# Optimization experiments

Hardware: AMD Instinct MI355X
Metric: run time of the kernel (lower is better)

Reference implementation:

```python
import jax, jax.numpy as jnp
import numpy as np

N_BITS = 8
QMAX = float(2 ** (N_BITS - 1) - 1)   # 127
QMIN = -QMAX - 1.0                     # -128
EPS = 1e-8


def _fq(x, scale):
    # symmetric fake quant: round, clamp, dequant
    return jnp.clip(jnp.round(x / scale), QMIN, QMAX) * scale


def fake_quant_per_token(x):
    # one scale per [..., :] vector (amax over last dim)
    max_abs = jnp.max(jnp.abs(x), axis=-1, keepdims=True)
    scale = jnp.maximum(max_abs / QMAX, EPS)
    return _fq(x, scale)


def fake_quant_per_channel(w):
    # w: [out, in]; ch_axis=0 -> one scale per output row (reduce over dim 1)
    max_abs = jnp.max(jnp.abs(w), axis=1, keepdims=True)
    scale = jnp.maximum(max_abs / QMAX, EPS)
    return _fq(w, scale)


def setup_inputs() -> dict:
    key = jax.random.key(0)
    kx, kw, kb = jax.random.split(key, 3)
    B, S, D_IN, D_OUT = 4, 2048, 4096, 4096
    x = jax.random.normal(kx, (B, S, D_IN), dtype=jnp.float32)
    w = jax.random.normal(kw, (D_OUT, D_IN), dtype=jnp.float32) * 0.02
    b = jax.random.normal(kb, (D_OUT,), dtype=jnp.float32) * 0.02
    return {"x": x, "w": w, "b": b}


def reference(x, w, b):
    # fake-quant path: W8 per-channel weight, A8 per-token activation
    w_q = fake_quant_per_channel(w)           # [O, I]
    x_q = fake_quant_per_token(x)             # [B, S, I]
    y = jnp.einsum('bsi,oi->bso', x_q, w_q) + b
    return y
```

## Files before the change

### kernel.cpp

```cpp
#include <hip/hip_runtime.h>
#include <hip/hip_bf16.h>


#define K_DIM 4096
#define N_DIM 4096
#define NT (K_DIM / 128)

typedef int v4i __attribute__((ext_vector_type(4)));

__device__ __forceinline__ void cp16(void* lds, const void* g) {
    __builtin_amdgcn_global_load_lds(
        (const __attribute__((address_space(1))) void*)g,
        (__attribute__((address_space(3))) void*)lds, 16, 0, 0);
}

__global__ __launch_bounds__(256) void quant_rows_kernel(
    const float* __restrict__ x, const float* __restrict__ w, int M,
    char* __restrict__ qx, char* __restrict__ qw,
    float* __restrict__ sx, float* __restrict__ sw) {
    const int blk = blockIdx.x;
    const bool is_x = blk < M;
    const int row = is_x ? blk : blk - M;
    const float* rp = (is_x ? x : w) + (size_t)row * 4096;
    char* qdst = is_x ? qx : qw;
    float* sdst = is_x ? sx : sw;

    const int tid = threadIdx.x;

    float4 v[4];
#pragma unroll
    for (int i = 0; i < 4; ++i)
        v[i] = *(const float4*)(rp + 4 * (tid + 256 * i));

    float m = 0.0f;
#pragma unroll
    for (int i = 0; i < 4; ++i) {
        m = fmaxf(m, fmaxf(fmaxf(fabsf(v[i].x), fabsf(v[i].y)),
                           fmaxf(fabsf(v[i].z), fabsf(v[i].w))));
    }
#pragma unroll
    for (int off = 32; off > 0; off >>= 1)
        m = fmaxf(m, __shfl_down(m, off));

    __shared__ float red[4];
    if ((tid & 63) == 0) red[tid >> 6] = m;
    __syncthreads();
    const float amax = fmaxf(fmaxf(red[0], red[1]), fmaxf(red[2], red[3]));
    const float scale = fmaxf(amax / 127.0f, 1e-8f);

    int* qout = (int*)(qdst + (size_t)row * 4096);
#pragma unroll
    for (int i = 0; i < 4; ++i) {
        int q0 = (int)fminf(fmaxf(rintf(v[i].x / scale), -128.0f), 127.0f);
        int q1 = (int)fminf(fmaxf(rintf(v[i].y / scale), -128.0f), 127.0f);
        int q2 = (int)fminf(fmaxf(rintf(v[i].z / scale), -128.0f), 127.0f);
        int q3 = (int)fminf(fmaxf(rintf(v[i].w / scale), -128.0f), 127.0f);
        qout[tid + 256 * i] =
            (q0 & 255) | ((q1 & 255) << 8) | ((q2 & 255) << 16) | ((q3 & 255) << 24);
    }
    if (tid == 0) sdst[row] = scale;
}

__global__ __launch_bounds__(512, 2) void gemm_i8_kernel(
    const char* __restrict__ qx, const char* __restrict__ qw,
    const float* __restrict__ sx, const float* __restrict__ sw,
    const float* __restrict__ bias, float* __restrict__ y) {

    __shared__ __align__(16) char lds[131072];

    const int tid  = threadIdx.x;
    const int wave = tid >> 6;
    const int lane = tid & 63;
    const int ln   = lane & 15;
    const int lg   = lane >> 4;
    const int wm   = wave >> 2;
    const int wn   = wave & 3;

    const int bm = blockIdx.y;
    const int bn = blockIdx.x;

    const int ci0 = tid,       r0s = ci0 >> 3, c0s = (ci0 & 7) ^ (r0s & 7);
    const int ci1 = tid + 512, r1s = ci1 >> 3, c1s = (ci1 & 7) ^ (r1s & 7);
    const char* aS0 = qx + (size_t)(bm * 256 + r0s) * K_DIM + c0s * 16;
    const char* aS1 = qx + (size_t)(bm * 256 + r1s) * K_DIM + c1s * 16;
    const char* bS0 = qw + (size_t)(bn * 256 + r0s) * K_DIM + c0s * 16;
    const char* bS1 = qw + (size_t)(bn * 256 + r1s) * K_DIM + c1s * 16;
    const int ldsC0 = ci0 * 16, ldsC1 = ci1 * 16;

#define SLOT_A(par, h) ((par) * 65536 + (h) * 16384)
#define SLOT_B(par, h) ((par) * 65536 + 32768 + (h) * 16384)
#define STAGE_A(par, h, t) do {                                              \
    cp16(lds + SLOT_A(par, h) + ldsC0,                                       \
         aS0 + (size_t)(h) * 128 * K_DIM + (size_t)(t) * 128);               \
    cp16(lds + SLOT_A(par, h) + ldsC1,                                       \
         aS1 + (size_t)(h) * 128 * K_DIM + (size_t)(t) * 128); } while (0)
#define STAGE_B(par, h, t) do {                                              \
    cp16(lds + SLOT_B(par, h) + ldsC0,                                       \
         bS0 + (size_t)(h) * 128 * K_DIM + (size_t)(t) * 128);               \
    cp16(lds + SLOT_B(par, h) + ldsC1,                                       \
         bS1 + (size_t)(h) * 128 * K_DIM + (size_t)(t) * 128); } while (0)

    const int ch0 = (lg ^ (ln & 7)) * 16;
    const int ch1 = ch0 ^ 64;
    const int aRd = wm * 16384 + ln * 128;
    const int bRd = 32768 + (wn >> 1) * 16384 + ((wn & 1) * 64 + ln) * 128;

    v4i acc[8][4] = {};

    STAGE_A(0, 0, 0); STAGE_A(0, 1, 0);
    STAGE_B(0, 0, 0); STAGE_B(0, 1, 0);
    STAGE_B(1, 0, 1); STAGE_B(1, 1, 1);
    asm volatile("s_waitcnt vmcnt(4)" ::: "memory");
    __builtin_amdgcn_s_barrier();
    asm volatile("" ::: "memory");

    for (int t = 0; t < NT; ++t) {
        const int par  = t & 1;
        const int base = par * 65536;
        v4i afr[4], bfr[4];

#pragma unroll
        for (int m = 0; m < 4; ++m)
            afr[m] = *(const v4i*)(lds + base + aRd + m * 2048 + ch0);
#pragma unroll
        for (int n = 0; n < 4; ++n)
            bfr[n] = *(const v4i*)(lds + base + bRd + n * 2048 + ch0);
        if (t + 1 < NT) STAGE_A(par ^ 1, 0, t + 1);
        __builtin_amdgcn_s_barrier();
        asm volatile("" ::: "memory");
        __builtin_amdgcn_s_setprio(1);
#pragma unroll
        for (int m = 0; m < 4; ++m)
#pragma unroll
            for (int n = 0; n < 4; ++n)
                acc[m][n] = __builtin_amdgcn_mfma_i32_16x16x64_i8(
                    afr[m], bfr[n], acc[m][n], 0, 0, 0);
        __builtin_amdgcn_s_setprio(0);
        __builtin_amdgcn_s_barrier();
        asm volatile("" ::: "memory");

#pragma unroll
        for (int m = 0; m < 4; ++m)
            afr[m] = *(const v4i*)(lds + base + aRd + (4 + m) * 2048 + ch0);
        if (t + 1 < NT) STAGE_A(par ^ 1, 1, t + 1);
        __builtin_amdgcn_s_barrier();
        asm volatile("" ::: "memory");
        __builtin_amdgcn_s_setprio(1);
#pragma unroll
        for (int m = 0; m < 4; ++m)
#pragma unroll
            for (int n = 0; n < 4; ++n)
                acc[4 + m][n] = __builtin_amdgcn_mfma_i32_16x16x64_i8(
                    afr[m], bfr[n], acc[4 + m][n], 0, 0, 0);
        __builtin_amdgcn_s_setprio(0);
        __builtin_amdgcn_s_barrier();
        asm volatile("" ::: "memory");

#pragma unroll
        for (int m = 0; m < 4; ++m)
            afr[m] = *(const v4i*)(lds + base + aRd + m * 2048 + ch1);
#pragma unroll
        for (int n = 0; n < 4; ++n)
            bfr[n] = *(const v4i*)(lds + base + bRd + n * 2048 + ch1);
        __builtin_amdgcn_s_barrier();
        asm volatile("" ::: "memory");
        __builtin_amdgcn_s_setprio(1);
#pragma unroll
        for (int m = 0; m < 4; ++m)
#pragma unroll
            for (int n = 0; n < 4; ++n)
                acc[m][n] = __builtin_amdgcn_mfma_i32_16x16x64_i8(
                    afr[m], bfr[n], acc[m][n], 0, 0, 0);
        __builtin_amdgcn_s_setprio(0);
        __builtin_amdgcn_s_barrier();
        asm volatile("" ::: "memory");

#pragma unroll
        for (int m = 0; m < 4; ++m)
            afr[m] = *(const v4i*)(lds + base + aRd + (4 + m) * 2048 + ch1);
        if (t + 2 < NT) { STAGE_B(par, 0, t + 2); STAGE_B(par, 1, t + 2); }
        __builtin_amdgcn_s_barrier();
        asm volatile("" ::: "memory");
        __builtin_amdgcn_s_setprio(1);
#pragma unroll
        for (int m = 0; m < 4; ++m)
#pragma unroll
            for (int n = 0; n < 4; ++n)
                acc[4 + m][n] = __builtin_amdgcn_mfma_i32_16x16x64_i8(
                    afr[m], bfr[n], acc[4 + m][n], 0, 0, 0);
        __builtin_amdgcn_s_setprio(0);
        if (t + 2 < NT)
            asm volatile("s_waitcnt vmcnt(4)" ::: "memory");
        else
            asm volatile("s_waitcnt vmcnt(0)" ::: "memory");
        __builtin_amdgcn_s_barrier();
        asm volatile("" ::: "memory");
    }

    const int m_base = bm * 256 + wm * 128;
    const int n_base = bn * 256 + wn * 64;

    float sxr[8][4];
#pragma unroll
    for (int m = 0; m < 8; ++m)
#pragma unroll
        for (int r = 0; r < 4; ++r)
            sxr[m][r] = sx[m_base + m * 16 + lg * 4 + r];

#pragma unroll
    for (int n = 0; n < 4; ++n) {
        const int col = n_base + n * 16 + ln;
        const float swv = sw[col];
        const float bv  = bias[col];
#pragma unroll
        for (int m = 0; m < 8; ++m) {
            const int row = m_base + m * 16 + lg * 4;
#pragma unroll
            for (int r = 0; r < 4; ++r) {
                y[(size_t)(row + r) * N_DIM + col] =
                    (float)acc[m][n][r] * sxr[m][r] * swv + bv;
            }
        }
    }
#undef SLOT_A
#undef SLOT_B
#undef STAGE_A
#undef STAGE_B
}

extern "C" void kernel_launch(void* const* d_in, const int* in_sizes, int n_in,
                              void* d_out, int out_size, void* d_ws, size_t ws_size,
                              hipStream_t stream) {
    const float* x = (const float*)d_in[0];
    const float* w = (const float*)d_in[1];
    const float* b = (const float*)d_in[2];
    float* y = (float*)d_out;

    const int M = in_sizes[0] / K_DIM;
    const int O = in_sizes[1] / K_DIM;

    char* qx = (char*)d_ws;
    char* qw = qx + (size_t)M * K_DIM;
    float* sx = (float*)(qw + (size_t)O * K_DIM);
    float* sw = sx + M;

    quant_rows_kernel<<<M + O, 256, 0, stream>>>(x, w, M, qx, qw, sx, sw);

    dim3 grid(N_DIM / 256, M / 256);
    gemm_i8_kernel<<<grid, 512, 0, stream>>>(qx, qw, sx, sw, b, y);
}
```

Baseline: 385.9 us.

## Restructure int8 GEMM main loop with register double-buffered fragments and swapped A/B prefetch

The main K loop is reorganised so LDS fragment reads for the next MFMA phase are issued before the current phase's MFMAs. The first fragment of the next tile is loaded at the end of the current iteration using separate aA/aB/b0/b1 register sets. The global-to-LDS prefetch is reordered: A is now prefetched two tiles ahead and B one tile ahead. sched_barrier calls pin instruction order around the barriers. This aims to hide LDS latency behind MFMA work, but adds register pressure and a full vmcnt(0) wait each iteration, which may expose global load latency.

```diff
diff --git a/kernel.cpp b/kernel.cpp
--- a/kernel.cpp
+++ b/kernel.cpp
@@ -100,101 +100,111 @@
     cp16(lds + SLOT_B(par, h) + ldsC1,                                       \
          bS1 + (size_t)(h) * 128 * K_DIM + (size_t)(t) * 128); } while (0)
 
+#define BAR()  __builtin_amdgcn_s_barrier()
+#define FENCE() asm volatile("" ::: "memory")
+#define SCHED() __builtin_amdgcn_sched_barrier(0)
+
     const int ch0 = (lg ^ (ln & 7)) * 16;
     const int ch1 = ch0 ^ 64;
     const int aRd = wm * 16384 + ln * 128;
     const int bRd = 32768 + (wn >> 1) * 16384 + ((wn & 1) * 64 + ln) * 128;
 
     v4i acc[8][4] = {};
+    v4i aA[4], aB[4], b0[4], b1[4];
 
     STAGE_A(0, 0, 0); STAGE_A(0, 1, 0);
     STAGE_B(0, 0, 0); STAGE_B(0, 1, 0);
-    STAGE_B(1, 0, 1); STAGE_B(1, 1, 1);
+    STAGE_A(1, 0, 1); STAGE_A(1, 1, 1);
     asm volatile("s_waitcnt vmcnt(4)" ::: "memory");
-    __builtin_amdgcn_s_barrier();
-    asm volatile("" ::: "memory");
+    BAR(); FENCE();
+#pragma unroll
+    for (int m = 0; m < 4; ++m)
+        aA[m] = *(const v4i*)(lds + aRd + m * 2048 + ch0);
+#pragma unroll
+    for (int n = 0; n < 4; ++n)
+        b0[n] = *(const v4i*)(lds + bRd + n * 2048 + ch0);
 
     for (int t = 0; t < NT; ++t) {
-        const int par  = t & 1;
-        const int base = par * 65536;
-        v4i afr[4], bfr[4];
-
-#pragma unroll
-        for (int m = 0; m < 4; ++m)
-            afr[m] = *(const v4i*)(lds + base + aRd + m * 2048 + ch0);
+        const int par   = t & 1;
+        const int base  = par << 16;
+        const int baseN = base ^ 65536;
+
+#pragma unroll
+        for (int m = 0; m < 4; ++m)
+            aB[m] = *(const v4i*)(lds + base + aRd + (4 + m) * 2048 + ch0);
+        if (t + 1 < NT) { STAGE_B(par ^ 1, 0, t + 1); STAGE_B(par ^ 1, 1, t + 1); }
+        SCHED();
+        BAR(); FENCE();
+        SCHED();
+        __builtin_amdgcn_s_setprio(1);
+#pragma unroll
+        for (int m = 0; m < 4; ++m)
+#pragma unroll
+            for (int n = 0; n < 4; ++n)
+                acc[m][n] = __builtin_amdgcn_mfma_i32_16x16x64_i8(
+                    aA[m], b0[n], acc[m][n], 0, 0, 0);
+        __builtin_amdgcn_s_setprio(0);
+        BAR(); FENCE();
+
+#pragma unroll
+        for (int m = 0; m < 4; ++m)
+            aA[m] = *(const v4i*)(lds + base + aRd + m * 2048 + ch1);
 #pragma unroll
         for (int n = 0; n < 4; ++n)
-            bfr[n] = *(const v4i*)(lds + base + bRd + n * 2048 + ch0);
-        if (t + 1 < NT) STAGE_A(par ^ 1, 0, t + 1);
-        __builtin_amdgcn_s_barrier();
-        asm volatile("" ::: "memory");
+            b1[n] = *(const v4i*)(lds + base + bRd + n * 2048 + ch1);
+        SCHED();
+        BAR(); FENCE();
+        SCHED();
+        __builtin_amdgcn_s_setprio(1);
+#pragma unroll
+        for (int m = 0; m < 4; ++m)
+#pragma unroll
+            for (int n = 0; n < 4; ++n)
+                acc[4 + m][n] = __builtin_amdgcn_mfma_i32_16x16x64_i8(
+                    aB[m], b0[n], acc[4 + m][n], 0, 0, 0);
+        __builtin_amdgcn_s_setprio(0);
+        BAR(); FENCE();
+
+#pragma unroll
+        for (int m = 0; m < 4; ++m)
+            aB[m] = *(const v4i*)(lds + base + aRd + (4 + m) * 2048 + ch1);
+        SCHED();
+        BAR(); FENCE();
+        SCHED();
         __builtin_amdgcn_s_setprio(1);
 #pragma unroll
         for (int m = 0; m < 4; ++m)
 #pragma unroll
             for (int n = 0; n < 4; ++n)
                 acc[m][n] = __builtin_amdgcn_mfma_i32_16x16x64_i8(
-                    afr[m], bfr[n], acc[m][n], 0, 0, 0);
-        __builtin_amdgcn_s_setprio(0);
-        __builtin_amdgcn_s_barrier();
-        asm volatile("" ::: "memory");
-
-#pragma unroll
-        for (int m = 0; m < 4; ++m)
-            afr[m] = *(const v4i*)(lds + base + aRd + (4 + m) * 2048 + ch0);
-        if (t + 1 < NT) STAGE_A(par ^ 1, 1, t + 1);
-        __builtin_amdgcn_s_barrier();
-        asm volatile("" ::: "memory");
+                    aA[m], b1[n], acc[m][n], 0, 0, 0);
+        __builtin_amdgcn_s_setprio(0);
+        asm volatile("s_waitcnt lgkmcnt(0)" ::: "memory");
+        asm volatile("s_waitcnt vmcnt(0)" ::: "memory");
+        BAR(); FENCE();
+
+        if (t + 1 < NT) {
+#pragma unroll
+            for (int m = 0; m < 4; ++m)
+                aA[m] = *(const v4i*)(lds + baseN + aRd + m * 2048 + ch0);
+#pragma unroll
+            for (int n = 0; n < 4; ++n)
+                b0[n] = *(const v4i*)(lds + baseN + bRd + n * 2048 + ch0);
+        }
+        SCHED();
+        BAR(); FENCE();
+        SCHED();
         __builtin_amdgcn_s_setprio(1);
 #pragma unroll
         for (int m = 0; m < 4; ++m)
 #pragma unroll
             for (int n = 0; n < 4; ++n)
                 acc[4 + m][n] = __builtin_amdgcn_mfma_i32_16x16x64_i8(
-                    afr[m], bfr[n], acc[4 + m][n], 0, 0, 0);
-        __builtin_amdgcn_s_setprio(0);
-        __builtin_amdgcn_s_barrier();
-        asm volatile("" ::: "memory");
-
-#pragma unroll
-        for (int m = 0; m < 4; ++m)
-            afr[m] = *(const v4i*)(lds + base + aRd + m * 2048 + ch1);
-#pragma unroll
-        for (int n = 0; n < 4; ++n)
-            bfr[n] = *(const v4i*)(lds + base + bRd + n * 2048 + ch1);
-        __builtin_amdgcn_s_barrier();
-        asm volatile("" ::: "memory");
-        __builtin_amdgcn_s_setprio(1);
-#pragma unroll
-        for (int m = 0; m < 4; ++m)
-#pragma unroll
-            for (int n = 0; n < 4; ++n)
-                acc[m][n] = __builtin_amdgcn_mfma_i32_16x16x64_i8(
-                    afr[m], bfr[n], acc[m][n], 0, 0, 0);
-        __builtin_amdgcn_s_setprio(0);
-        __builtin_amdgcn_s_barrier();
-        asm volatile("" ::: "memory");
-
-#pragma unroll
-        for (int m = 0; m < 4; ++m)
-            afr[m] = *(const v4i*)(lds + base + aRd + (4 + m) * 2048 + ch1);
-        if (t + 2 < NT) { STAGE_B(par, 0, t + 2); STAGE_B(par, 1, t + 2); }
-        __builtin_amdgcn_s_barrier();
-        asm volatile("" ::: "memory");
-        __builtin_amdgcn_s_setprio(1);
-#pragma unroll
-        for (int m = 0; m < 4; ++m)
-#pragma unroll
-            for (int n = 0; n < 4; ++n)
-                acc[4 + m][n] = __builtin_amdgcn_mfma_i32_16x16x64_i8(
-                    afr[m], bfr[n], acc[4 + m][n], 0, 0, 0);
-        __builtin_amdgcn_s_setprio(0);
-        if (t + 2 < NT)
-            asm volatile("s_waitcnt vmcnt(4)" ::: "memory");
-        else
-            asm volatile("s_waitcnt vmcnt(0)" ::: "memory");
-        __builtin_amdgcn_s_barrier();
-        asm volatile("" ::: "memory");
+                    aB[m], b1[n], acc[4 + m][n], 0, 0, 0);
+        __builtin_amdgcn_s_setprio(0);
+        if (t + 2 < NT) { STAGE_A(par, 0, t + 2); STAGE_A(par, 1, t + 2); }
+        SCHED();
+        BAR(); FENCE();
     }
 
     const int m_base = bm * 256 + wm * 128;
@@ -226,6 +236,9 @@
 #undef SLOT_B
 #undef STAGE_A
 #undef STAGE_B
+#undef BAR
+#undef FENCE
+#undef SCHED
 }
 
 extern "C" void kernel_launch(void* const* d_in, const int* in_sizes, int n_in,
```

After: 389.2 us. No clear change (+0.8%).

## Restructure int8 GEMM main loop into two phases with single-stage prefetch

Applied to the files above, without the earlier changes.

Each K tile now runs as two phases over the full 8x4 fragment block instead of four half-M phases. All 8 A fragments are loaded at once, which removes per-tile barriers. B staging changes from a two-tile lookahead into the same parity to a one-tile prefetch into the opposite buffer, issued alongside the second half. A vmcnt(0) wait now ends every iteration. This lowers barrier count and gives larger MFMA bursts, but costs more live registers and less load latency hiding, since B for t+1 is issued only midway through tile t. The B read offset formula is also changed to a simpler per-wave layout.

```diff
diff --git a/kernel.cpp b/kernel.cpp
--- a/kernel.cpp
+++ b/kernel.cpp
@@ -100,101 +100,62 @@
     cp16(lds + SLOT_B(par, h) + ldsC1,                                       \
          bS1 + (size_t)(h) * 128 * K_DIM + (size_t)(t) * 128); } while (0)
 
+#define BAR()   __builtin_amdgcn_s_barrier()
+#define FENCE() asm volatile("" ::: "memory")
+
     const int ch0 = (lg ^ (ln & 7)) * 16;
     const int ch1 = ch0 ^ 64;
     const int aRd = wm * 16384 + ln * 128;
-    const int bRd = 32768 + (wn >> 1) * 16384 + ((wn & 1) * 64 + ln) * 128;
+    const int bRd = 32768 + wn * 8192 + ln * 128;
 
     v4i acc[8][4] = {};
 
     STAGE_A(0, 0, 0); STAGE_A(0, 1, 0);
     STAGE_B(0, 0, 0); STAGE_B(0, 1, 0);
-    STAGE_B(1, 0, 1); STAGE_B(1, 1, 1);
-    asm volatile("s_waitcnt vmcnt(4)" ::: "memory");
-    __builtin_amdgcn_s_barrier();
-    asm volatile("" ::: "memory");
+    asm volatile("s_waitcnt vmcnt(0)" ::: "memory");
+    BAR(); FENCE();
 
     for (int t = 0; t < NT; ++t) {
         const int par  = t & 1;
-        const int base = par * 65536;
-        v4i afr[4], bfr[4];
-
-#pragma unroll
-        for (int m = 0; m < 4; ++m)
+        const int base = par << 16;
+        v4i afr[8], bfr[4];
+
+#pragma unroll
+        for (int m = 0; m < 8; ++m)
             afr[m] = *(const v4i*)(lds + base + aRd + m * 2048 + ch0);
 #pragma unroll
         for (int n = 0; n < 4; ++n)
             bfr[n] = *(const v4i*)(lds + base + bRd + n * 2048 + ch0);
-        if (t + 1 < NT) STAGE_A(par ^ 1, 0, t + 1);
-        __builtin_amdgcn_s_barrier();
-        asm volatile("" ::: "memory");
+        if (t + 1 < NT) { STAGE_A(par ^ 1, 0, t + 1); STAGE_A(par ^ 1, 1, t + 1); }
+        BAR(); FENCE();
         __builtin_amdgcn_s_setprio(1);
 #pragma unroll
-        for (int m = 0; m < 4; ++m)
+        for (int m = 0; m < 8; ++m)
 #pragma unroll
             for (int n = 0; n < 4; ++n)
                 acc[m][n] = __builtin_amdgcn_mfma_i32_16x16x64_i8(
                     afr[m], bfr[n], acc[m][n], 0, 0, 0);
         __builtin_amdgcn_s_setprio(0);
-        __builtin_amdgcn_s_barrier();
-        asm volatile("" ::: "memory");
-
-#pragma unroll
-        for (int m = 0; m < 4; ++m)
-            afr[m] = *(const v4i*)(lds + base + aRd + (4 + m) * 2048 + ch0);
-        if (t + 1 < NT) STAGE_A(par ^ 1, 1, t + 1);
-        __builtin_amdgcn_s_barrier();
-        asm volatile("" ::: "memory");
-        __builtin_amdgcn_s_setprio(1);
-#pragma unroll
-        for (int m = 0; m < 4; ++m)
-#pragma unroll
-            for (int n = 0; n < 4; ++n)
-                acc[4 + m][n] = __builtin_amdgcn_mfma_i32_16x16x64_i8(
-                    afr[m], bfr[n], acc[4 + m][n], 0, 0, 0);
-        __builtin_amdgcn_s_setprio(0);
-        __builtin_amdgcn_s_barrier();
-        asm volatile("" ::: "memory");
-
-#pragma unroll
-        for (int m = 0; m < 4; ++m)
+        BAR(); FENCE();
+
+#pragma unroll
+        for (int m = 0; m < 8; ++m)
             afr[m] = *(const v4i*)(lds + base + aRd + m * 2048 + ch1);
 #pragma unroll
         for (int n = 0; n < 4; ++n)
             bfr[n] = *(const v4i*)(lds + base + bRd + n * 2048 + ch1);
-        __builtin_amdgcn_s_barrier();
-        asm volatile("" ::: "memory");
+        if (t + 1 < NT) { STAGE_B(par ^ 1, 0, t + 1); STAGE_B(par ^ 1, 1, t + 1); }
+        BAR(); FENCE();
         __builtin_amdgcn_s_setprio(1);
 #pragma unroll
-        for (int m = 0; m < 4; ++m)
+        for (int m = 0; m < 8; ++m)
 #pragma unroll
             for (int n = 0; n < 4; ++n)
                 acc[m][n] = __builtin_amdgcn_mfma_i32_16x16x64_i8(
                     afr[m], bfr[n], acc[m][n], 0, 0, 0);
         __builtin_amdgcn_s_setprio(0);
-        __builtin_amdgcn_s_barrier();
-        asm volatile("" ::: "memory");
-
-#pragma unroll
-        for (int m = 0; m < 4; ++m)
-            afr[m] = *(const v4i*)(lds + base + aRd + (4 + m) * 2048 + ch1);
-        if (t + 2 < NT) { STAGE_B(par, 0, t + 2); STAGE_B(par, 1, t + 2); }
-        __builtin_amdgcn_s_barrier();
-        asm volatile("" ::: "memory");
-        __builtin_amdgcn_s_setprio(1);
-#pragma unroll
-        for (int m = 0; m < 4; ++m)
-#pragma unroll
-            for (int n = 0; n < 4; ++n)
-                acc[4 + m][n] = __builtin_amdgcn_mfma_i32_16x16x64_i8(
-                    afr[m], bfr[n], acc[4 + m][n], 0, 0, 0);
-        __builtin_amdgcn_s_setprio(0);
-        if (t + 2 < NT)
-            asm volatile("s_waitcnt vmcnt(4)" ::: "memory");
-        else
-            asm volatile("s_waitcnt vmcnt(0)" ::: "memory");
-        __builtin_amdgcn_s_barrier();
-        asm volatile("" ::: "memory");
+        asm volatile("s_waitcnt vmcnt(0)" ::: "memory");
+        BAR(); FENCE();
     }
 
     const int m_base = bm * 256 + wm * 128;
@@ -226,6 +187,8 @@
 #undef SLOT_B
 #undef STAGE_A
 #undef STAGE_B
+#undef BAR
+#undef FENCE
 }
 
 extern "C" void kernel_launch(void* const* d_in, const int* in_sizes, int n_in,
```

Result: no change. 384.5 us (-0.4%).
